# Kernel optimization log

Hardware: AMD Instinct MI355X
Metric: run time of the kernel (lower is better)

The kernel has to match this reference:

```python
import jax, jax.numpy as jnp
import numpy as np


def setup_inputs() -> dict:
    key = jax.random.key(0)
    ks = jax.random.split(key, 8)
    T, S, W, O = 50000, 168, 336, 48
    N = T - W - O + 1
    x = jax.random.uniform(ks[0], (T,), minval=0.5, maxval=1.5, dtype=jnp.float32)
    noise = jax.random.normal(ks[1], (N, W), dtype=jnp.float32) * 0.001  # Normal(0, std=0.001)
    level_sc = jax.random.uniform(ks[2], (), minval=-1.0, maxval=1.0, dtype=jnp.float32)
    seas_sc = jax.random.uniform(ks[3], (), minval=-1.0, maxval=1.0, dtype=jnp.float32)
    init_seas = jax.random.uniform(ks[4], (S,), minval=0.65, maxval=1.35, dtype=jnp.float32)
    W1 = jax.random.normal(ks[5], (W, W), dtype=jnp.float32) / np.float32(np.sqrt(W))
    b1 = jnp.zeros((W,), jnp.float32)
    W2 = jax.random.normal(ks[6], (W, O), dtype=jnp.float32) / np.float32(np.sqrt(W))
    b2 = jnp.zeros((O,), jnp.float32)
    return {"x": x, "noise": noise, "level_sc": level_sc, "seas_sc": seas_sc,
            "init_seas": init_seas, "W1": W1, "b1": b1, "W2": W2, "b2": b2,
            "window_size": W, "out_size": O, "lvp": 1}


def reference(x, noise, level_sc, seas_sc, init_seas, W1, b1, W2, b2,
              window_size, out_size, lvp):
    T = x.shape[0]
    a = jax.nn.sigmoid(level_sc)      # level smoothing coeff
    g = jax.nn.sigmoid(seas_sc)       # seasonal smoothing coeff
    s0 = jnp.exp(init_seas)           # [S] initial multiplicative seasonals
    # seasonals list in torch: seas[0..S-1]=s0, seas[S]=s0[0], seas[S+i]=w_i.
    # Ring buffer holds seas[i..i+S-1] at step i (starting i=1): [s0[1:], s0[0]].
    buf0 = jnp.concatenate([s0[1:], s0[:1]])
    level0 = x[0] / s0[0]

    def step(carry, xi):
        level, buf = carry
        seas_i = buf[0]
        new_level = a * xi / seas_i + (1.0 - a) * level
        new_w = g * xi / new_level + (1.0 - g) * seas_i
        new_buf = jnp.concatenate([buf[1:], new_w[None]])
        return (new_level, new_buf), (new_level, new_w, jnp.log(new_level / level))

    _, (lvls, ws, logdiffs) = jax.lax.scan(step, (level0, buf0), x[1:])
    levels = jnp.concatenate([level0[None], lvls])        # [T]
    seas_full = jnp.concatenate([s0, s0[:1], ws])         # [S+T]

    d = logdiffs[1:] - logdiffs[:-1]
    level_var_loss = jnp.mean(d * d) * lvp

    N = T - window_size - out_size + 1
    idx_in = jnp.arange(N)[:, None] + jnp.arange(window_size)[None, :]   # [N,W]
    idx_lab = jnp.arange(N)[:, None] + window_size + jnp.arange(out_size)[None, :]  # [N,O]
    lev = levels[jnp.arange(N) + window_size][:, None]    # [N,1]
    inp = jnp.log(x[idx_in] / (lev * seas_full[idx_in])) + noise   # noisy squashed inputs
    labels = jnp.log(x[idx_lab] / (lev * seas_full[idx_lab]))

    h = jnp.tanh(inp @ W1 + b1)        # tanh_no_lstm: Linear(336,336)+tanh
    out = h @ W2 + b2                  # linear_no_lstm: Linear(336,48)
    return out, labels, level_var_loss
```

## Files before the change

kernel.cpp:

```cpp
#include <hip/hip_runtime.h>

typedef __attribute__((ext_vector_type(8))) short  s16x8;
typedef __attribute__((ext_vector_type(4))) short  s16x4;
typedef __attribute__((ext_vector_type(4))) float  f32x4;

#define T_LEN 50000
#define S_LEN 168
#define W_IN  336
#define O_OUT 48
#define N_ROWS (T_LEN - W_IN - O_OUT + 1)
#define N_PAD  49664
#define NBLK   (N_PAD / 64)

__device__ inline short f2bf(float f) {
    union { float f; unsigned u; } v; v.f = f;
    unsigned u = v.u;
    unsigned r = u + 0x7fffu + ((u >> 16) & 1u);
    return (short)(r >> 16);
}

__device__ inline float readlane_f(float v, int l) {
    return __int_as_float(__builtin_amdgcn_readlane(__float_as_int(v), l));
}

__device__ inline float fast_tanh(float v) {
    float e = __expf(2.f * v);
    return 1.f - 2.f * __builtin_amdgcn_rcpf(e + 1.f);
}

__global__ void k_preconvert(const float* __restrict__ W1, const float* __restrict__ W2,
                             short* __restrict__ W1T, short* __restrict__ W2T) {
    int idx = blockIdx.x * 256 + threadIdx.x;
    const int n1 = 352 * 352;
    const int tot = n1 + 48 * 360;
    if (idx >= tot) return;
    if (idx < n1) {
        int j = idx / 352, k = idx % 352;
        W1T[idx] = (j < 336 && k < 336) ? f2bf(W1[k * 336 + j]) : (short)0;
    } else {
        int i2 = idx - n1;
        int o = i2 / 360, k = i2 % 360;
        W2T[i2] = (k < 336) ? f2bf(W2[k * 48 + o]) : (short)0;
    }
}

#define DPP_STEP(q_, CTRL, OMW) { \
    int t_ = __builtin_amdgcn_update_dpp(0, __float_as_int(q_), (CTRL), 0xf, 0xf, true); \
    q_ = fmaf((OMW), __int_as_float(t_), q_); }

__global__ void k_scan(const float* __restrict__ x, const float* __restrict__ level_sc,
                       const float* __restrict__ seas_sc, const float* __restrict__ init_seas,
                       float* __restrict__ levels, float* __restrict__ seas_full) {
    __shared__ float ring[256];
    int lane = threadIdx.x;
    float a = 1.f / (1.f + expf(-level_sc[0]));
    float g = 1.f / (1.f + expf(-seas_sc[0]));
    float om = 1.f - a, omg = 1.f - g;

    for (int t = lane; t < 256; t += 64) {
        float s = 1.f;
        if (t <= S_LEN) { s = expf(init_seas[t < S_LEN ? t : 0]); seas_full[t] = s; }
        ring[t] = s;
    }
    float lpv = x[0] / expf(init_seas[0]);
    if (lane == 0) levels[0] = lpv;
    __syncthreads();

    float om1 = om, om2v = om1 * om1, om4 = om2v * om2v, om8 = om4 * om4, om16 = om8 * om8;
    float pl   = powf(om, (float)(lane + 1));
    float fpre = powf(om, (float)((lane & 15) + 1));
    bool isr1 = (lane >> 4) == 1, isr2 = (lane >> 4) == 2, isr3 = (lane >> 4) == 3;

#define SCAN(QOUT, XV, RSV) { \
    float q_ = a * (XV) * (RSV); \
    DPP_STEP(q_, 0x111, om1); \
    DPP_STEP(q_, 0x112, om2v); \
    DPP_STEP(q_, 0x114, om4); \
    DPP_STEP(q_, 0x118, om8); \
    float e0_ = readlane_f(q_, 15); \
    float e1_ = readlane_f(q_, 31); \
    float e2_ = readlane_f(q_, 47); \
    float t2_ = fmaf(om16, e0_, e1_); \
    float t3_ = fmaf(om16, t2_, e2_); \
    float pre_ = isr1 ? e0_ : (isr2 ? t2_ : (isr3 ? t3_ : 0.f)); \
    QOUT = fmaf(fpre, pre_, q_); }

#define XLOAD(I) float xr##I = x[1 + 64 * I + lane];
    XLOAD(0) XLOAD(1) XLOAD(2) XLOAD(3) XLOAD(4) XLOAD(5) XLOAD(6) XLOAD(7)
    XLOAD(8) XLOAD(9) XLOAD(10) XLOAD(11) XLOAD(12) XLOAD(13) XLOAD(14) XLOAD(15)
#undef XLOAD

    float sA0 = ring[1 + lane];
    float Qcur; SCAN(Qcur, xr0, __builtin_amdgcn_rcpf(sA0));
    float sW = sA0;
    float ldsA = ring[65 + lane];
    float ldsB;
    int ib = 1;

#define BODY(R, RN, LIN, LOUT) { \
    float lvl = fmaf(pl, lpv, Qcur); \
    lpv = readlane_f(lvl, 63); \
    levels[ib + lane] = lvl; \
    float w_ = fmaf(omg, sW, (g * xr##R) * __builtin_amdgcn_rcpf(lvl)); \
    seas_full[S_LEN + ib + lane] = w_; \
    ring[(ib + S_LEN + lane) & 255] = w_; \
    LOUT = ring[(ib + 128 + lane) & 255]; \
    float rsn_ = __builtin_amdgcn_rcpf(LIN); \
    float Qn_; SCAN(Qn_, xr##RN, rsn_); \
    int pidx = ib + 1024 + lane; pidx = pidx > (T_LEN - 1) ? (T_LEN - 1) : pidx; \
    xr##R = x[pidx]; \
    Qcur = Qn_; sW = LIN; \
    ib += 64; }

    for (int kb = 0; kb < 48; ++kb) {
        BODY(0,1,  ldsA, ldsB) BODY(1,2,  ldsB, ldsA) BODY(2,3,  ldsA, ldsB) BODY(3,4,  ldsB, ldsA)
        BODY(4,5,  ldsA, ldsB) BODY(5,6,  ldsB, ldsA) BODY(6,7,  ldsA, ldsB) BODY(7,8,  ldsB, ldsA)
        BODY(8,9,  ldsA, ldsB) BODY(9,10, ldsB, ldsA) BODY(10,11,ldsA, ldsB) BODY(11,12,ldsB, ldsA)
        BODY(12,13,ldsA, ldsB) BODY(13,14,ldsB, ldsA) BODY(14,15,ldsA, ldsB) BODY(15,0, ldsB, ldsA)
    }
    BODY(0,1,  ldsA, ldsB) BODY(1,2,  ldsB, ldsA) BODY(2,3,  ldsA, ldsB) BODY(3,4,  ldsB, ldsA)
    BODY(4,5,  ldsA, ldsB) BODY(5,6,  ldsB, ldsA) BODY(6,7,  ldsA, ldsB) BODY(7,8,  ldsB, ldsA)
    BODY(8,9,  ldsA, ldsB) BODY(9,10, ldsB, ldsA) BODY(10,11,ldsA, ldsB) BODY(11,12,ldsB, ldsA)
#undef BODY

    {
        float lvl = fmaf(pl, lpv, Qcur);
        lpv = readlane_f(lvl, 63);
        levels[49921 + lane] = lvl;
        float w_ = fmaf(omg, sW, (g * xr12) * __builtin_amdgcn_rcpf(lvl));
        seas_full[S_LEN + 49921 + lane] = w_;
    }
    {
        float rsn_ = __builtin_amdgcn_rcpf(ldsA);
        float Qn_; SCAN(Qn_, xr13, rsn_);
        float lvl = fmaf(pl, lpv, Qn_);
        if (lane < 15) {
            levels[49985 + lane] = lvl;
            float w_ = fmaf(omg, ldsA, (g * xr13) * __builtin_amdgcn_rcpf(lvl));
            seas_full[S_LEN + 49985 + lane] = w_;
        }
    }
#undef SCAN
}

__global__ void k_logs(const float* __restrict__ x, const float* __restrict__ levels,
                       const float* __restrict__ seas_full,
                       float* __restrict__ F, float* __restrict__ llev,
                       float* __restrict__ partials) {
    __shared__ float sm[258];
    __shared__ float red[256];
    int tid = threadIdx.x;
    int t = blockIdx.x * 256 + tid;
    float ll = 0.f;
    if (t < T_LEN) {
        F[t]  = __logf(x[t]) - __logf(seas_full[t]);
        ll    = __logf(levels[t]);
        llev[t] = ll;
    }
    sm[tid] = ll;
    if (tid < 2) {
        int te = blockIdx.x * 256 + 256 + tid;
        sm[256 + tid] = (te < T_LEN) ? __logf(levels[te]) : 0.f;
    }
    __syncthreads();
    float s = 0.f;
    if (t < T_LEN - 2) {
        float d = sm[tid + 2] - 2.f * sm[tid + 1] + sm[tid];
        s = d * d;
    }
    red[tid] = s; __syncthreads();
    for (int off = 128; off > 0; off >>= 1) {
        if (tid < off) red[tid] += red[tid + off];
        __syncthreads();
    }
    if (tid == 0) partials[blockIdx.x] = red[0];
}

__global__ __launch_bounds__(256, 3) void k_gemm(
        const float* __restrict__ noise, const float* __restrict__ F,
        const float* __restrict__ llev, const short* __restrict__ W1T,
        const float* __restrict__ b1, const short* __restrict__ W2T,
        const float* __restrict__ b2, const float* __restrict__ partials,
        const int* __restrict__ lvp, float* __restrict__ out,
        float* __restrict__ labels, float* __restrict__ loss) {
    __shared__ __align__(16) short Bb[2][352 * 36];
    __shared__ __align__(16) float Flds[448];
    __shared__ __align__(16) float Llds[64];
    __shared__ __align__(16) float b1lds[352];

    int t = threadIdx.x, w = t >> 6, l = t & 63;
    int lm = l & 15, lq = l >> 4;
    long n0 = (long)blockIdx.x * 64;

    if (blockIdx.x == 0 && w == 3) {
        float s = partials[l] + partials[l + 64] + partials[l + 128];
        if (l < 4) s += partials[l + 192];
#pragma unroll
        for (int off = 32; off > 0; off >>= 1) s += __shfl_down(s, off, 64);
        if (l == 0) loss[0] = s / (float)(T_LEN - 2) * (float)lvp[0];
    }

    if (t < 112)      *(f32x4*)&Flds[t * 4] = *(const f32x4*)&F[n0 + t * 4];
    else if (t < 128) *(f32x4*)&Llds[(t - 112) * 4] = *(const f32x4*)&llev[n0 + W_IN + (t - 112) * 4];
    else if (t < 216) {
        int i4 = (t - 128) * 4;
        f32x4 v = (f32x4){0.f, 0.f, 0.f, 0.f};
        if (i4 < W_IN) v = *(const f32x4*)&b1[i4];
        *(f32x4*)&b1lds[i4] = v;
    }
#pragma unroll
    for (int it = 0; it < 6; ++it) {
        int q = t + it * 256;
        if (q < 1408) {
            int j = q >> 2, kc = q & 3;
            s16x8 v = *(const s16x8*)&W1T[j * 352 + kc * 8];
            *(s16x4*)&Bb[0][j * 36 + kc * 8]     = (s16x4){v[0], v[1], v[2], v[3]};
            *(s16x4*)&Bb[0][j * 36 + kc * 8 + 4] = (s16x4){v[4], v[5], v[6], v[7]};
        }
    }

    int rbase = (w >> 1) * 32;
    int jbase = (w & 1) * 176;
    long an0 = n0 + rbase + lm, an1 = an0 + 16;
    const long amax = (long)N_ROWS * W_IN - 8;
    long a00 = an0 * W_IN, a10 = an1 * W_IN;

    long p0 = a00 + lq * 8; if (p0 > amax) p0 = amax;
    long p1 = a10 + lq * 8; if (p1 > amax) p1 = amax;
    f32x4 nc00 = *(const f32x4*)&noise[p0], nc01 = *(const f32x4*)&noise[p0 + 4];
    f32x4 nc10 = *(const f32x4*)&noise[p1], nc11 = *(const f32x4*)&noise[p1 + 4];

    f32x4 acc0[11], acc1[11];
#pragma unroll
    for (int c = 0; c < 11; ++c) { acc0[c] = (f32x4){0,0,0,0}; acc1[c] = (f32x4){0,0,0,0}; }

    __syncthreads();
    float lv0 = Llds[rbase + lm], lv1 = Llds[rbase + 16 + lm];

#pragma unroll
    for (int ks = 0; ks < 11; ++ks) {
        s16x8 wr0, wr1, wr2, wr3, wr4, wr5;
        if (ks < 10) {
            int ko = (ks + 1) * 32;
            wr0 = *(const s16x8*)&W1T[((t       ) >> 2) * 352 + ko + ((t       ) & 3) * 8];
            wr1 = *(const s16x8*)&W1T[((t +  256) >> 2) * 352 + ko + ((t +  256) & 3) * 8];
            wr2 = *(const s16x8*)&W1T[((t +  512) >> 2) * 352 + ko + ((t +  512) & 3) * 8];
            wr3 = *(const s16x8*)&W1T[((t +  768) >> 2) * 352 + ko + ((t +  768) & 3) * 8];
            wr4 = *(const s16x8*)&W1T[((t + 1024) >> 2) * 352 + ko + ((t + 1024) & 3) * 8];
            if (t < 128)
                wr5 = *(const s16x8*)&W1T[((t + 1280) >> 2) * 352 + ko + ((t + 1280) & 3) * 8];
        }
        f32x4 nn00, nn01, nn10, nn11;
        if (ks < 10) {
            int kb = (ks + 1) * 32 + lq * 8;
            long q0 = a00 + kb; if (q0 > amax) q0 = amax;
            long q1 = a10 + kb; if (q1 > amax) q1 = amax;
            nn00 = *(const f32x4*)&noise[q0]; nn01 = *(const f32x4*)&noise[q0 + 4];
            nn10 = *(const f32x4*)&noise[q1]; nn11 = *(const f32x4*)&noise[q1 + 4];
        }
        int fb = rbase + lm + ks * 32 + lq * 8;
        s16x8 bf0, bf1;
#pragma unroll
        for (int j = 0; j < 8; ++j) {
            float nv0 = (j < 4) ? nc00[j] : nc01[j - 4];
            float nv1 = (j < 4) ? nc10[j] : nc11[j - 4];
            bf0[j] = f2bf(Flds[fb + j]      - lv0 + nv0);
            bf1[j] = f2bf(Flds[fb + 16 + j] - lv1 + nv1);
        }
#pragma unroll
        for (int ct = 0; ct < 11; ++ct) {
            int bo = (jbase + ct * 16 + lm) * 36 + lq * 8;
            s16x4 afl = *(s16x4*)&Bb[ks & 1][bo];
            s16x4 afh = *(s16x4*)&Bb[ks & 1][bo + 4];
            s16x8 af = (s16x8){afl[0], afl[1], afl[2], afl[3], afh[0], afh[1], afh[2], afh[3]};
            acc0[ct] = __builtin_amdgcn_mfma_f32_16x16x32_bf16(af, bf0, acc0[ct], 0, 0, 0);
            acc1[ct] = __builtin_amdgcn_mfma_f32_16x16x32_bf16(af, bf1, acc1[ct], 0, 0, 0);
        }
        if (ks < 10) {
            int nb = (ks + 1) & 1;
#define WST(WR, OFS) { if ((OFS) < 1280 || t < 128) { int q = t + (OFS); int j = q >> 2, kc = q & 3; \
            *(s16x4*)&Bb[nb][j * 36 + kc * 8]     = (s16x4){WR[0], WR[1], WR[2], WR[3]}; \
            *(s16x4*)&Bb[nb][j * 36 + kc * 8 + 4] = (s16x4){WR[4], WR[5], WR[6], WR[7]}; } }
            WST(wr0, 0) WST(wr1, 256) WST(wr2, 512) WST(wr3, 768) WST(wr4, 1024) WST(wr5, 1280)
#undef WST
            nc00 = nn00; nc01 = nn01; nc10 = nn10; nc11 = nn11;
        }
        __syncthreads();
    }

    short (*hlds)[360] = (short(*)[360])&Bb[0][0];
#pragma unroll
    for (int ct = 0; ct < 11; ++ct) {
        f32x4 b1q = *(f32x4*)&b1lds[jbase + ct * 16 + lq * 4];
        s16x4 h0, h1;
#pragma unroll
        for (int r = 0; r < 4; ++r) {
            h0[r] = f2bf(fast_tanh(acc0[ct][r] + b1q[r]));
            h1[r] = f2bf(fast_tanh(acc1[ct][r] + b1q[r]));
        }
        *(s16x4*)&hlds[rbase + lm][jbase + ct * 16 + lq * 4]      = h0;
        *(s16x4*)&hlds[rbase + 16 + lm][jbase + ct * 16 + lq * 4] = h1;
    }
    __syncthreads();

    f32x4 a2[3];
    a2[0] = (f32x4){0,0,0,0}; a2[1] = (f32x4){0,0,0,0}; a2[2] = (f32x4){0,0,0,0};
#pragma unroll
    for (int ks = 0; ks < 11; ++ks) {
        s16x8 af2 = *(s16x8*)&hlds[w * 16 + lm][ks * 32 + lq * 8];
#pragma unroll
        for (int ct = 0; ct < 3; ++ct) {
            s16x8 bf2 = *(const s16x8*)&W2T[(ct * 16 + lm) * 360 + ks * 32 + lq * 8];
            a2[ct] = __builtin_amdgcn_mfma_f32_16x16x32_bf16(af2, bf2, a2[ct], 0, 0, 0);
        }
    }

    int rloc = w * 16 + lq * 4;
#pragma unroll
    for (int ct = 0; ct < 3; ++ct) {
        float b2v = b2[ct * 16 + lm];
#pragma unroll
        for (int r = 0; r < 4; ++r) {
            long row = n0 + rloc + r;
            if (row < N_ROWS) {
                int col = ct * 16 + lm;
                out[row * O_OUT + col]    = a2[ct][r] + b2v;
                labels[row * O_OUT + col] = Flds[rloc + r + W_IN + col] - Llds[rloc + r];
            }
        }
    }
}

extern "C" void kernel_launch(void* const* d_in, const int* in_sizes, int n_in,
                              void* d_out, int out_size, void* d_ws, size_t ws_size,
                              hipStream_t stream) {
    const float* x         = (const float*)d_in[0];
    const float* noise     = (const float*)d_in[1];
    const float* level_sc  = (const float*)d_in[2];
    const float* seas_sc   = (const float*)d_in[3];
    const float* init_seas = (const float*)d_in[4];
    const float* W1        = (const float*)d_in[5];
    const float* b1        = (const float*)d_in[6];
    const float* W2        = (const float*)d_in[7];
    const float* b2        = (const float*)d_in[8];
    const int*   lvp       = (const int*)d_in[11];

    float* out    = (float*)d_out;
    float* labels = out + (long)N_ROWS * O_OUT;
    float* loss   = labels + (long)N_ROWS * O_OUT;

    float* wsf       = (float*)d_ws;
    float* levels    = wsf;
    float* seas_full = wsf + 50048;
    float* F         = wsf + 100224;
    float* llev      = wsf + 150400;
    float* partials  = wsf + 200448;
    short* W1T       = (short*)(wsf + 200704);
    short* W2T       = W1T + 352 * 352;

    k_preconvert<<<552, 256, 0, stream>>>(W1, W2, W1T, W2T);
    k_scan<<<1, 64, 0, stream>>>(x, level_sc, seas_sc, init_seas, levels, seas_full);
    k_logs<<<196, 256, 0, stream>>>(x, levels, seas_full, F, llev, partials);
    k_gemm<<<NBLK, 256, 0, stream>>>(noise, F, llev, W1T, b1, W2T, b2,
                                     partials, lvp, out, labels, loss);
}
```

Before: 168.4 us.

## Load W1 fragments directly from global memory instead of staging through LDS

Removes the double-buffered LDS staging of W1T along with its per-k-step barriers. Each wave now loads its MFMA A-fragments for all 11 column tiles straight from global (L2-cached) memory every k-step, and the k loop is no longer unrolled. This drops the LDS store/load traffic and the __syncthreads calls, and it shrinks shared memory so more blocks may fit per CU. In exchange, every wave re-fetches W1 from cache with no reuse across the waves in a block, and the loads are no longer prefetched a step ahead, so latency may be exposed.

Result: slower. 172.9 us (+2.7%).

```diff
diff --git a/kernel.cpp b/kernel.cpp
--- a/kernel.cpp
+++ b/kernel.cpp
@@ -183,7 +183,7 @@
         const float* __restrict__ b2, const float* __restrict__ partials,
         const int* __restrict__ lvp, float* __restrict__ out,
         float* __restrict__ labels, float* __restrict__ loss) {
-    __shared__ __align__(16) short Bb[2][352 * 36];
+    __shared__ __align__(16) short hlds[64][360];
     __shared__ __align__(16) float Flds[448];
     __shared__ __align__(16) float Llds[64];
     __shared__ __align__(16) float b1lds[352];
@@ -208,16 +208,6 @@
         if (i4 < W_IN) v = *(const f32x4*)&b1[i4];
         *(f32x4*)&b1lds[i4] = v;
     }
-#pragma unroll
-    for (int it = 0; it < 6; ++it) {
-        int q = t + it * 256;
-        if (q < 1408) {
-            int j = q >> 2, kc = q & 3;
-            s16x8 v = *(const s16x8*)&W1T[j * 352 + kc * 8];
-            *(s16x4*)&Bb[0][j * 36 + kc * 8]     = (s16x4){v[0], v[1], v[2], v[3]};
-            *(s16x4*)&Bb[0][j * 36 + kc * 8 + 4] = (s16x4){v[4], v[5], v[6], v[7]};
-        }
-    }
 
     int rbase = (w >> 1) * 32;
     int jbase = (w & 1) * 176;
@@ -237,19 +227,13 @@
     __syncthreads();
     float lv0 = Llds[rbase + lm], lv1 = Llds[rbase + 16 + lm];
 
-#pragma unroll
+    const short* w1row = &W1T[(jbase + lm) * 352 + lq * 8];
+#pragma unroll 1
     for (int ks = 0; ks < 11; ++ks) {
-        s16x8 wr0, wr1, wr2, wr3, wr4, wr5;
-        if (ks < 10) {
-            int ko = (ks + 1) * 32;
-            wr0 = *(const s16x8*)&W1T[((t       ) >> 2) * 352 + ko + ((t       ) & 3) * 8];
-            wr1 = *(const s16x8*)&W1T[((t +  256) >> 2) * 352 + ko + ((t +  256) & 3) * 8];
-            wr2 = *(const s16x8*)&W1T[((t +  512) >> 2) * 352 + ko + ((t +  512) & 3) * 8];
-            wr3 = *(const s16x8*)&W1T[((t +  768) >> 2) * 352 + ko + ((t +  768) & 3) * 8];
-            wr4 = *(const s16x8*)&W1T[((t + 1024) >> 2) * 352 + ko + ((t + 1024) & 3) * 8];
-            if (t < 128)
-                wr5 = *(const s16x8*)&W1T[((t + 1280) >> 2) * 352 + ko + ((t + 1280) & 3) * 8];
-        }
+        s16x8 af[11];
+#pragma unroll
+        for (int ct = 0; ct < 11; ++ct)
+            af[ct] = *(const s16x8*)&w1row[ct * 16 * 352 + ks * 32];
         f32x4 nn00, nn01, nn10, nn11;
         if (ks < 10) {
             int kb = (ks + 1) * 32 + lq * 8;
@@ -269,26 +253,12 @@
         }
 #pragma unroll
         for (int ct = 0; ct < 11; ++ct) {
-            int bo = (jbase + ct * 16 + lm) * 36 + lq * 8;
-            s16x4 afl = *(s16x4*)&Bb[ks & 1][bo];
-            s16x4 afh = *(s16x4*)&Bb[ks & 1][bo + 4];
-            s16x8 af = (s16x8){afl[0], afl[1], afl[2], afl[3], afh[0], afh[1], afh[2], afh[3]};
-            acc0[ct] = __builtin_amdgcn_mfma_f32_16x16x32_bf16(af, bf0, acc0[ct], 0, 0, 0);
-            acc1[ct] = __builtin_amdgcn_mfma_f32_16x16x32_bf16(af, bf1, acc1[ct], 0, 0, 0);
-        }
-        if (ks < 10) {
-            int nb = (ks + 1) & 1;
-#define WST(WR, OFS) { if ((OFS) < 1280 || t < 128) { int q = t + (OFS); int j = q >> 2, kc = q & 3; \
-            *(s16x4*)&Bb[nb][j * 36 + kc * 8]     = (s16x4){WR[0], WR[1], WR[2], WR[3]}; \
-            *(s16x4*)&Bb[nb][j * 36 + kc * 8 + 4] = (s16x4){WR[4], WR[5], WR[6], WR[7]}; } }
-            WST(wr0, 0) WST(wr1, 256) WST(wr2, 512) WST(wr3, 768) WST(wr4, 1024) WST(wr5, 1280)
-#undef WST
-            nc00 = nn00; nc01 = nn01; nc10 = nn10; nc11 = nn11;
-        }
-        __syncthreads();
-    }
-
-    short (*hlds)[360] = (short(*)[360])&Bb[0][0];
+            acc0[ct] = __builtin_amdgcn_mfma_f32_16x16x32_bf16(af[ct], bf0, acc0[ct], 0, 0, 0);
+            acc1[ct] = __builtin_amdgcn_mfma_f32_16x16x32_bf16(af[ct], bf1, acc1[ct], 0, 0, 0);
+        }
+        nc00 = nn00; nc01 = nn01; nc10 = nn10; nc11 = nn11;
+    }
+
 #pragma unroll
     for (int ct = 0; ct < 11; ++ct) {
         f32x4 b1q = *(f32x4*)&b1lds[jbase + ct * 16 + lq * 4];
```
